# Kernel tuning notes

Measured on AMD Instinct MI355X. Metric: run time of the kernel, lower is better.

Reference implementation:

```python
import jax, jax.numpy as jnp
import numpy as np

K = 16          # number of nearest neighbors (init kwarg k)
EPS = 1e-3      # denom threshold from the original code


def setup_inputs() -> dict:
    key = jax.random.key(0)
    k1, k2, k3 = jax.random.split(key, 3)
    V, F = 5000, 10000
    vertices = jax.random.normal(k1, (V, 3), dtype=jnp.float32)
    faces = jax.random.randint(k2, (F, 3), 0, V)
    probabilities = jax.random.uniform(k3, (F,), dtype=jnp.float32)
    return {"vertices": vertices, "faces": faces, "probabilities": probabilities}


def reference(vertices, faces, probabilities):
    F = faces.shape[0]
    pos = vertices[faces]                       # [F,3,3] triangle vertex coords
    bary = pos.mean(axis=1)                     # [F,3] barycenters

    # brute-force kNN over barycenters (x == y, so self is included like torch_geometric knn)
    sq = jnp.sum(bary * bary, axis=-1)          # [F]
    d2 = sq[:, None] + sq[None, :] - 2.0 * (bary @ bary.T)   # [F,F]
    _, nbr = jax.lax.top_k(-d2, K)              # [F,K] neighbor face indices

    # face normals
    e1 = pos[:, 1] - pos[:, 0]
    e2 = pos[:, 2] - pos[:, 0]
    n = jnp.cross(e1, e2)
    n = n / jnp.maximum(jnp.linalg.norm(n, axis=-1, keepdims=True), 1e-12)  # [F,3]

    # per (tri, neighbor, triangle-edge) plane intersection test
    nb_pos = pos[nbr]                           # [F,K,3,3] neighbor triangle vertices
    l0 = nb_pos                                 # segment starts
    l1 = jnp.roll(nb_pos, -1, axis=2)           # segment ends (k -> (k+1)%3)
    n_b = n[:, None, None, :]                   # [F,1,1,3]
    p0_b = pos[:, 0][:, None, None, :]          # [F,1,1,3] plane point of tri

    denom = jnp.sum(n_b * (l1 - l0), axis=-1)   # [F,K,3]
    numer = jnp.sum(n_b * (p0_b - l0), axis=-1) # [F,K,3]
    safe_denom = jnp.where(jnp.abs(denom) < EPS, 1.0, denom)
    t = numer / safe_denom
    hit = (jnp.abs(denom) >= EPS) & (t > 0.0) & (t < 1.0)   # [F,K,3]

    # early break in original => at most 1 increment per (tri, neighbor) pair
    pen = jnp.any(hit, axis=-1) & (nbr != jnp.arange(F)[:, None])  # [F,K]

    # scatter-add penetrations into neighbor_idx
    faces_penetrated = jnp.zeros((F,), jnp.float32).at[nbr.ravel()].add(
        pen.ravel().astype(jnp.float32))

    return jnp.dot(probabilities, faces_penetrated) / F
```

## Files before the change

### kernel.cpp

```cpp
#include <hip/hip_runtime.h>
#include <math.h>

#define KNN 16
#define EPS_F 0.001f
#define BLK 256
#define LCAP 17
#define SCH 16
#define SSTRIDE 8

#define REP16(M) M(0) M(1) M(2) M(3) M(4) M(5) M(6) M(7) \
                 M(8) M(9) M(10) M(11) M(12) M(13) M(14) M(15)

#define CEAI(p,a,b) { int _lo = min(p##a, p##b); int _hi = max(p##a, p##b); p##a = _lo; p##b = _hi; }
#define CEDI(p,a,b) { int _lo = min(p##a, p##b); int _hi = max(p##a, p##b); p##a = _hi; p##b = _lo; }

#define SORT16I(p) \
  CEAI(p,0,1) CEDI(p,2,3) CEAI(p,4,5) CEDI(p,6,7) CEAI(p,8,9) CEDI(p,10,11) CEAI(p,12,13) CEDI(p,14,15) \
  CEAI(p,0,2) CEAI(p,1,3) CEDI(p,4,6) CEDI(p,5,7) CEAI(p,8,10) CEAI(p,9,11) CEDI(p,12,14) CEDI(p,13,15) \
  CEAI(p,0,1) CEAI(p,2,3) CEDI(p,4,5) CEDI(p,6,7) CEAI(p,8,9) CEAI(p,10,11) CEDI(p,12,13) CEDI(p,14,15) \
  CEAI(p,0,4) CEAI(p,1,5) CEAI(p,2,6) CEAI(p,3,7) CEDI(p,8,12) CEDI(p,9,13) CEDI(p,10,14) CEDI(p,11,15) \
  CEAI(p,0,2) CEAI(p,1,3) CEAI(p,4,6) CEAI(p,5,7) CEDI(p,8,10) CEDI(p,9,11) CEDI(p,12,14) CEDI(p,13,15) \
  CEAI(p,0,1) CEAI(p,2,3) CEAI(p,4,5) CEAI(p,6,7) CEDI(p,8,9) CEDI(p,10,11) CEDI(p,12,13) CEDI(p,14,15) \
  CEAI(p,0,8) CEAI(p,1,9) CEAI(p,2,10) CEAI(p,3,11) CEAI(p,4,12) CEAI(p,5,13) CEAI(p,6,14) CEAI(p,7,15) \
  CEAI(p,0,4) CEAI(p,1,5) CEAI(p,2,6) CEAI(p,3,7) CEAI(p,8,12) CEAI(p,9,13) CEAI(p,10,14) CEAI(p,11,15) \
  CEAI(p,0,2) CEAI(p,1,3) CEAI(p,4,6) CEAI(p,5,7) CEAI(p,8,10) CEAI(p,9,11) CEAI(p,12,14) CEAI(p,13,15) \
  CEAI(p,0,1) CEAI(p,2,3) CEAI(p,4,5) CEAI(p,6,7) CEAI(p,8,9) CEAI(p,10,11) CEAI(p,12,13) CEAI(p,14,15)

#define RESORT16I(p) \
  CEAI(p,0,8) CEAI(p,1,9) CEAI(p,2,10) CEAI(p,3,11) CEAI(p,4,12) CEAI(p,5,13) CEAI(p,6,14) CEAI(p,7,15) \
  CEAI(p,0,4) CEAI(p,1,5) CEAI(p,2,6) CEAI(p,3,7) CEAI(p,8,12) CEAI(p,9,13) CEAI(p,10,14) CEAI(p,11,15) \
  CEAI(p,0,2) CEAI(p,1,3) CEAI(p,4,6) CEAI(p,5,7) CEAI(p,8,10) CEAI(p,9,11) CEAI(p,12,14) CEAI(p,13,15) \
  CEAI(p,0,1) CEAI(p,2,3) CEAI(p,4,5) CEAI(p,6,7) CEAI(p,8,9) CEAI(p,10,11) CEAI(p,12,13) CEAI(p,14,15)

#define MERGE16I(r,x) \
  r##0=min(r##0,x##15); r##1=min(r##1,x##14); r##2=min(r##2,x##13); r##3=min(r##3,x##12); \
  r##4=min(r##4,x##11); r##5=min(r##5,x##10); r##6=min(r##6,x##9);  r##7=min(r##7,x##8);  \
  r##8=min(r##8,x##7);  r##9=min(r##9,x##6);  r##10=min(r##10,x##5); r##11=min(r##11,x##4); \
  r##12=min(r##12,x##3); r##13=min(r##13,x##2); r##14=min(r##14,x##1); r##15=min(r##15,x##0); \
  RESORT16I(r)

__device__ __forceinline__ float distf(float4 q, float4 P) {
    return fmaf(q.x, P.x, fmaf(q.y, P.y, fmaf(q.z, P.z, q.w + P.w)));
}
__device__ __forceinline__ int packkey(float d2, int j) {
    return (__float_as_int(d2) & 0xFFFFC000) | j;
}

__global__ __launch_bounds__(BLK) void prep_kernel(
    const float* __restrict__ verts, const int* __restrict__ faces,
    float4* __restrict__ baryq, float4* __restrict__ baryqm,
    float* __restrict__ nrm, float* __restrict__ p0s, int F)
{
    int f = blockIdx.x * BLK + threadIdx.x;
    if (f >= F) return;
    int i0 = faces[3*f+0], i1 = faces[3*f+1], i2 = faces[3*f+2];
    float ax = verts[3*i0+0], ay = verts[3*i0+1], az = verts[3*i0+2];
    float bx = verts[3*i1+0], by = verts[3*i1+1], bz = verts[3*i1+2];
    float cx = verts[3*i2+0], cy = verts[3*i2+1], cz = verts[3*i2+2];
    float gx = (ax + bx + cx) / 3.0f;
    float gy = (ay + by + cy) / 3.0f;
    float gz = (az + bz + cz) / 3.0f;
    float sq = gx*gx + gy*gy + gz*gz;
    baryq[f]  = make_float4(gx, gy, gz, sq);
    baryqm[f] = make_float4(-2.0f*gx, -2.0f*gy, -2.0f*gz, sq);
    float e1x = bx-ax, e1y = by-ay, e1z = bz-az;
    float e2x = cx-ax, e2y = cy-ay, e2z = cz-az;
    float nx = e1y*e2z - e1z*e2y;
    float ny = e1z*e2x - e1x*e2z;
    float nz = e1x*e2y - e1y*e2x;
    float len = sqrtf(nx*nx + ny*ny + nz*nz);
    float dn = fmaxf(len, 1e-12f);
    nrm[3*f+0] = nx/dn; nrm[3*f+1] = ny/dn; nrm[3*f+2] = nz/dn;
    p0s[3*f+0] = ax; p0s[3*f+1] = ay; p0s[3*f+2] = az;
}

__global__ __launch_bounds__(BLK) void knn_sample(
    const float4* __restrict__ baryq, const float4* __restrict__ baryqm,
    int* __restrict__ samp_k, int F, int SLEN)
{
    int tid = threadIdx.x;
    int qi = blockIdx.x * BLK + tid;
    float4 q = baryq[min(qi, F-1)];
    #define DECLR(m) int r##m = 0x7fffffff;
    REP16(DECLR)
    #undef DECLR
    int sbase = blockIdx.y * SLEN;
    #pragma unroll 1
    for (int g = 0; g < SLEN; g += 16) {
        #define MKK(m) int x##m; { int s = sbase + g + (m); int j = s * SSTRIDE; \
            float4 P = baryqm[min(j, F-1)]; \
            int k = packkey(distf(q, P), j); \
            x##m = (j < F) ? k : 0x7fffffff; }
        REP16(MKK)
        #undef MKK
        SORT16I(x)
        MERGE16I(r, x)
    }
    if (qi < F) {
        size_t cb = (size_t)blockIdx.y * KNN * F + qi;
        #define STR(m) samp_k[cb + (size_t)(m) * F] = r##m;
        REP16(STR)
        #undef STR
    }
}

__global__ __launch_bounds__(BLK) void merge_T(
    const int* __restrict__ samp_k, int* __restrict__ Tkey,
    int* __restrict__ cnt, int F)
{
    int qi = blockIdx.x * BLK + threadIdx.x;
    if (qi >= F) return;
    #define LDR(m) int r##m = samp_k[(size_t)(m) * F + qi];
    REP16(LDR)
    #undef LDR
    for (int c = 1; c < SCH; ++c) {
        size_t cb = (size_t)c * KNN * F + qi;
        #define LDX(m) int x##m = samp_k[cb + (size_t)(m) * F];
        REP16(LDX)
        #undef LDX
        MERGE16I(r, x)
    }
    Tkey[qi] = r15;
    cnt[qi] = 0;
}

__global__ __launch_bounds__(BLK, 8) void collect_kernel(
    const float4* __restrict__ baryq, const float4* __restrict__ baryqm,
    const int* __restrict__ Tkey, int* __restrict__ cnt,
    int* __restrict__ buf, int F, int CLEN, int CAP)
{
    __shared__ int lb[BLK * LCAP];
    int tid = threadIdx.x;
    int qi = blockIdx.x * BLK + tid;
    bool active = qi < F;
    int qc = min(qi, F-1);
    float4 q = baryq[qc];
    int T = active ? Tkey[qc] : 0x80000000;
    int lbb = tid * LCAP;
    int lcnt = 0;
    int jb = blockIdx.y * CLEN;
    int je = min(jb + CLEN, F);
    int jfull = jb + ((je - jb) & ~15);
    #pragma unroll 1
    for (int base = jb; base < jfull; base += 16) {
        const float4* tp = baryqm + base;
        #define CSTEP(m) { float4 P = tp[m]; \
            int key = packkey(distf(q, P), base + (m)); \
            if (key <= T) { lb[lbb + min(lcnt, LCAP-1)] = key; ++lcnt; } }
        REP16(CSTEP)
        #undef CSTEP
    }
    for (int j = jfull; j < je; ++j) {
        float4 P = baryqm[j];
        int key = packkey(distf(q, P), j);
        if (key <= T) { lb[lbb + min(lcnt, LCAP-1)] = key; ++lcnt; }
    }
    lcnt = min(lcnt, LCAP);
    if (active && lcnt > 0) {
        int basep = atomicAdd(&cnt[qi], lcnt);
        for (int k = 0; k < lcnt; ++k) {
            int p = basep + k;
            if (p < CAP) buf[(size_t)qi * CAP + p] = lb[lbb + k];
        }
    }
}

__device__ __forceinline__ bool edge_test(
    float nx, float ny, float nz, float px, float py, float pz,
    float ax, float ay, float az, float bx, float by, float bz)
{
    float denom = nx*(bx-ax) + ny*(by-ay) + nz*(bz-az);
    if (fabsf(denom) < EPS_F) return false;
    float numer = nx*(px-ax) + ny*(py-ay) + nz*(pz-az);
    float t = numer / denom;
    return (t > 0.0f) && (t < 1.0f);
}

__global__ __launch_bounds__(BLK) void select_pen(
    const int* __restrict__ buf, const int* __restrict__ cnt,
    const float* __restrict__ verts, const int* __restrict__ faces,
    const float* __restrict__ prob, const float* __restrict__ nrm,
    const float* __restrict__ p0s, float* __restrict__ partial,
    int F, int CAP)
{
    int qi = blockIdx.x * BLK + threadIdx.x;
    float val = 0.0f;
    if (qi < F) {
        int n = min(cnt[qi], CAP);
        const int* row = buf + (size_t)qi * CAP;
        #define DECLR(m) int r##m = 0x7fffffff;
        REP16(DECLR)
        #undef DECLR
        #pragma unroll 1
        for (int t = 0; t < n; t += 16) {
            #define LSEL(m) int x##m; { int v = row[t + (m)]; \
                x##m = (t + (m) < n) ? v : 0x7fffffff; }
            REP16(LSEL)
            #undef LSEL
            SORT16I(x)
            MERGE16I(r, x)
        }
        float nx = nrm[3*qi+0], ny = nrm[3*qi+1], nz = nrm[3*qi+2];
        float px = p0s[3*qi+0], py = p0s[3*qi+1], pz = p0s[3*qi+2];
        #define PENM(m) { int j = r##m & 0x3FFF; \
            if (j != qi && j < F) { \
                int j0 = faces[3*j+0], j1 = faces[3*j+1], j2 = faces[3*j+2]; \
                float ax = verts[3*j0+0], ay = verts[3*j0+1], az = verts[3*j0+2]; \
                float bx = verts[3*j1+0], by = verts[3*j1+1], bz = verts[3*j1+2]; \
                float cx = verts[3*j2+0], cy = verts[3*j2+1], cz = verts[3*j2+2]; \
                bool hit = edge_test(nx,ny,nz, px,py,pz, ax,ay,az, bx,by,bz) \
                        || edge_test(nx,ny,nz, px,py,pz, bx,by,bz, cx,cy,cz) \
                        || edge_test(nx,ny,nz, px,py,pz, cx,cy,cz, ax,ay,az); \
                if (hit) val += prob[j]; } }
        REP16(PENM)
        #undef PENM
    }
    __shared__ float red[BLK];
    red[threadIdx.x] = val;
    __syncthreads();
    #pragma unroll
    for (int s = BLK/2; s > 0; s >>= 1) {
        if (threadIdx.x < s) red[threadIdx.x] += red[threadIdx.x + s];
        __syncthreads();
    }
    if (threadIdx.x == 0) partial[blockIdx.x] = red[0];
}

__global__ __launch_bounds__(BLK) void final_reduce(
    const float* __restrict__ partial, int n, float* __restrict__ out, int F)
{
    __shared__ float red[BLK];
    float s = 0.0f;
    for (int i = threadIdx.x; i < n; i += BLK) s += partial[i];
    red[threadIdx.x] = s;
    __syncthreads();
    #pragma unroll
    for (int st = BLK/2; st > 0; st >>= 1) {
        if (threadIdx.x < st) red[threadIdx.x] += red[threadIdx.x + st];
        __syncthreads();
    }
    if (threadIdx.x == 0) out[0] = red[0] / (float)F;
}

extern "C" void kernel_launch(void* const* d_in, const int* in_sizes, int n_in,
                              void* d_out, int out_size, void* d_ws, size_t ws_size,
                              hipStream_t stream)
{
    const float* verts = (const float*)d_in[0];
    const int*   faces = (const int*)d_in[1];
    const float* prob  = (const float*)d_in[2];
    float* out = (float*)d_out;
    int F = in_sizes[2];

    size_t off = 0;
    auto carve = [&](size_t bytes) {
        size_t cur = off;
        off += (bytes + 255) & ~(size_t)255;
        return cur;
    };
    char* w = (char*)d_ws;
    int qBlocks = (F + BLK - 1) / BLK;
    float4* baryq  = (float4*)(w + carve((size_t)F * sizeof(float4)));
    float4* baryqm = (float4*)(w + carve((size_t)F * sizeof(float4)));
    float*  nrm    = (float*)(w + carve((size_t)F * 3 * sizeof(float)));
    float*  p0s    = (float*)(w + carve((size_t)F * 3 * sizeof(float)));
    float*  partial= (float*)(w + carve((size_t)qBlocks * sizeof(float)));
    int*    Tkey   = (int*)(w + carve((size_t)F * sizeof(int)));
    int*    cnt    = (int*)(w + carve((size_t)F * sizeof(int)));
    int*    samp_k = (int*)(w + carve((size_t)SCH * KNN * F * sizeof(int)));

    size_t remain = (ws_size > off) ? (ws_size - off) : 0;
    int CAP = (int)(remain / ((size_t)F * sizeof(int)));
    if (CAP > 448) CAP = 448;
    if (CAP < 320) CAP = 320;
    CAP &= ~15;
    int* buf = (int*)(w + carve((size_t)F * CAP * sizeof(int)));

    int nSamp = (F + SSTRIDE - 1) / SSTRIDE;
    int SLEN = ((nSamp + SCH - 1) / SCH + 15) & ~15;
    int CCH = 80;
    int CLEN = (((F + CCH - 1) / CCH) + 15) & ~15;
    int nCChunk = (F + CLEN - 1) / CLEN;

    prep_kernel<<<qBlocks, BLK, 0, stream>>>(verts, faces, baryq, baryqm, nrm, p0s, F);
    knn_sample<<<dim3(qBlocks, SCH), BLK, 0, stream>>>(baryq, baryqm, samp_k, F, SLEN);
    merge_T<<<qBlocks, BLK, 0, stream>>>(samp_k, Tkey, cnt, F);
    collect_kernel<<<dim3(qBlocks, nCChunk), BLK, 0, stream>>>(
        baryq, baryqm, Tkey, cnt, buf, F, CLEN, CAP);
    select_pen<<<qBlocks, BLK, 0, stream>>>(
        buf, cnt, verts, faces, prob, nrm, p0s, partial, F, CAP);
    final_reduce<<<1, BLK, 0, stream>>>(partial, qBlocks, out, F);
}
```

Baseline: 99.38 us.

## Stage kNN samples in LDS, use per-hit atomics, drop final reduce kernel

knn_sample now stages its strided sample barycenters in dynamic shared memory and pads the out-of-range ones with infinity, so the per-iteration global loads and clamps go away. collect_kernel drops the per-thread LDS staging buffer, which raises occupancy, and does a global atomicAdd per candidate instead. The final_reduce launch is removed: out is zeroed in merge_T and select_pen atomically adds its block sums. The chunk count for collect is now derived from a target of about 2048 blocks. Per-hit atomics add contention on cnt, and the float atomic sum makes the result order-dependent.

```diff
diff --git a/kernel.cpp b/kernel.cpp
--- a/kernel.cpp
+++ b/kernel.cpp
@@ -4,7 +4,6 @@
 #define KNN 16
 #define EPS_F 0.001f
 #define BLK 256
-#define LCAP 17
 #define SCH 16
 #define SSTRIDE 8
 
@@ -78,6 +77,7 @@
     const float4* __restrict__ baryq, const float4* __restrict__ baryqm,
     int* __restrict__ samp_k, int F, int SLEN)
 {
+    extern __shared__ float4 sb[];
     int tid = threadIdx.x;
     int qi = blockIdx.x * BLK + tid;
     float4 q = baryq[min(qi, F-1)];
@@ -85,12 +85,14 @@
     REP16(DECLR)
     #undef DECLR
     int sbase = blockIdx.y * SLEN;
+    if (tid < SLEN) {
+        int j = (sbase + tid) * SSTRIDE;
+        sb[tid] = (j < F) ? baryqm[j] : make_float4(0.f, 0.f, 0.f, INFINITY);
+    }
+    __syncthreads();
     #pragma unroll 1
     for (int g = 0; g < SLEN; g += 16) {
-        #define MKK(m) int x##m; { int s = sbase + g + (m); int j = s * SSTRIDE; \
-            float4 P = baryqm[min(j, F-1)]; \
-            int k = packkey(distf(q, P), j); \
-            x##m = (j < F) ? k : 0x7fffffff; }
+        #define MKK(m) int x##m = packkey(distf(q, sb[g+(m)]), (sbase+g+(m))*SSTRIDE);
         REP16(MKK)
         #undef MKK
         SORT16I(x)
@@ -106,9 +108,10 @@
 
 __global__ __launch_bounds__(BLK) void merge_T(
     const int* __restrict__ samp_k, int* __restrict__ Tkey,
-    int* __restrict__ cnt, int F)
+    int* __restrict__ cnt, float* __restrict__ out, int F)
 {
     int qi = blockIdx.x * BLK + threadIdx.x;
+    if (blockIdx.x == 0 && threadIdx.x == 0) out[0] = 0.0f;
     if (qi >= F) return;
     #define LDR(m) int r##m = samp_k[(size_t)(m) * F + qi];
     REP16(LDR)
@@ -129,15 +132,12 @@
     const int* __restrict__ Tkey, int* __restrict__ cnt,
     int* __restrict__ buf, int F, int CLEN, int CAP)
 {
-    __shared__ int lb[BLK * LCAP];
     int tid = threadIdx.x;
     int qi = blockIdx.x * BLK + tid;
     bool active = qi < F;
     int qc = min(qi, F-1);
     float4 q = baryq[qc];
     int T = active ? Tkey[qc] : 0x80000000;
-    int lbb = tid * LCAP;
-    int lcnt = 0;
     int jb = blockIdx.y * CLEN;
     int je = min(jb + CLEN, F);
     int jfull = jb + ((je - jb) & ~15);
@@ -146,21 +146,18 @@
         const float4* tp = baryqm + base;
         #define CSTEP(m) { float4 P = tp[m]; \
             int key = packkey(distf(q, P), base + (m)); \
-            if (key <= T) { lb[lbb + min(lcnt, LCAP-1)] = key; ++lcnt; } }
+            if (key <= T) { \
+                int pos = atomicAdd(&cnt[qi], 1); \
+                if (pos < CAP) buf[(size_t)qi * CAP + pos] = key; } }
         REP16(CSTEP)
         #undef CSTEP
     }
     for (int j = jfull; j < je; ++j) {
         float4 P = baryqm[j];
         int key = packkey(distf(q, P), j);
-        if (key <= T) { lb[lbb + min(lcnt, LCAP-1)] = key; ++lcnt; }
-    }
-    lcnt = min(lcnt, LCAP);
-    if (active && lcnt > 0) {
-        int basep = atomicAdd(&cnt[qi], lcnt);
-        for (int k = 0; k < lcnt; ++k) {
-            int p = basep + k;
-            if (p < CAP) buf[(size_t)qi * CAP + p] = lb[lbb + k];
+        if (key <= T) {
+            int pos = atomicAdd(&cnt[qi], 1);
+            if (pos < CAP) buf[(size_t)qi * CAP + pos] = key;
         }
     }
 }
@@ -180,7 +177,7 @@
     const int* __restrict__ buf, const int* __restrict__ cnt,
     const float* __restrict__ verts, const int* __restrict__ faces,
     const float* __restrict__ prob, const float* __restrict__ nrm,
-    const float* __restrict__ p0s, float* __restrict__ partial,
+    const float* __restrict__ p0s, float* __restrict__ out,
     int F, int CAP)
 {
     int qi = blockIdx.x * BLK + threadIdx.x;
@@ -223,23 +220,7 @@
         if (threadIdx.x < s) red[threadIdx.x] += red[threadIdx.x + s];
         __syncthreads();
     }
-    if (threadIdx.x == 0) partial[blockIdx.x] = red[0];
-}
-
-__global__ __launch_bounds__(BLK) void final_reduce(
-    const float* __restrict__ partial, int n, float* __restrict__ out, int F)
-{
-    __shared__ float red[BLK];
-    float s = 0.0f;
-    for (int i = threadIdx.x; i < n; i += BLK) s += partial[i];
-    red[threadIdx.x] = s;
-    __syncthreads();
-    #pragma unroll
-    for (int st = BLK/2; st > 0; st >>= 1) {
-        if (threadIdx.x < st) red[threadIdx.x] += red[threadIdx.x + st];
-        __syncthreads();
-    }
-    if (threadIdx.x == 0) out[0] = red[0] / (float)F;
+    if (threadIdx.x == 0) atomicAdd(out, red[0] / (float)F);
 }
 
 extern "C" void kernel_launch(void* const* d_in, const int* in_sizes, int n_in,
@@ -264,30 +245,29 @@
     float4* baryqm = (float4*)(w + carve((size_t)F * sizeof(float4)));
     float*  nrm    = (float*)(w + carve((size_t)F * 3 * sizeof(float)));
     float*  p0s    = (float*)(w + carve((size_t)F * 3 * sizeof(float)));
-    float*  partial= (float*)(w + carve((size_t)qBlocks * sizeof(float)));
     int*    Tkey   = (int*)(w + carve((size_t)F * sizeof(int)));
     int*    cnt    = (int*)(w + carve((size_t)F * sizeof(int)));
     int*    samp_k = (int*)(w + carve((size_t)SCH * KNN * F * sizeof(int)));
 
     size_t remain = (ws_size > off) ? (ws_size - off) : 0;
-    int CAP = (int)(remain / ((size_t)F * sizeof(int)));
+    int CAP = (int)((remain - 256) / ((size_t)F * sizeof(int)));
     if (CAP > 448) CAP = 448;
     if (CAP < 320) CAP = 320;
     CAP &= ~15;
-    int* buf = (int*)(w + carve((size_t)F * CAP * sizeof(int)));
+    int* buf = (int*)(w + carve((size_t)F * CAP * sizeof(int) + 256));
 
     int nSamp = (F + SSTRIDE - 1) / SSTRIDE;
     int SLEN = ((nSamp + SCH - 1) / SCH + 15) & ~15;
-    int CCH = 80;
-    int CLEN = (((F + CCH - 1) / CCH) + 15) & ~15;
+    int nChTarget = (2048 / qBlocks > 1) ? (2048 / qBlocks) : 1;
+    int CLEN = (((F + nChTarget - 1) / nChTarget) + 15) & ~15;
     int nCChunk = (F + CLEN - 1) / CLEN;
 
     prep_kernel<<<qBlocks, BLK, 0, stream>>>(verts, faces, baryq, baryqm, nrm, p0s, F);
-    knn_sample<<<dim3(qBlocks, SCH), BLK, 0, stream>>>(baryq, baryqm, samp_k, F, SLEN);
-    merge_T<<<qBlocks, BLK, 0, stream>>>(samp_k, Tkey, cnt, F);
+    knn_sample<<<dim3(qBlocks, SCH), BLK, SLEN * sizeof(float4), stream>>>(
+        baryq, baryqm, samp_k, F, SLEN);
+    merge_T<<<qBlocks, BLK, 0, stream>>>(samp_k, Tkey, cnt, out, F);
     collect_kernel<<<dim3(qBlocks, nCChunk), BLK, 0, stream>>>(
         baryq, baryqm, Tkey, cnt, buf, F, CLEN, CAP);
     select_pen<<<qBlocks, BLK, 0, stream>>>(
-        buf, cnt, verts, faces, prob, nrm, p0s, partial, F, CAP);
-    final_reduce<<<1, BLK, 0, stream>>>(partial, qBlocks, out, F);
-}
+        buf, cnt, verts, faces, prob, nrm, p0s, out, F, CAP);
+}
```

Result: slower. 152.6 us (+53.6%).
